# Kernel tuning notes

Measured on AMD Instinct MI355X. Metric: run time of the kernel, lower is better.

Reference implementation:

```python
import jax, jax.numpy as jnp
import numpy as np

H, NH, KVH = 2048, 16, 4
HD = H // NH            # 128
GROUPS = NH // KVH      # 4
E, TOPK = 8, 2
I_MOE, I_SH = 1408, 5632
THETA = 1000000.0
EPS = 1e-6
B, S = 1, 1024


def rms_norm(x, w):
    var = jnp.mean(jnp.square(x), axis=-1, keepdims=True)
    return x * jax.lax.rsqrt(var + EPS) * w


def rotate_half(x):
    x1, x2 = jnp.split(x, 2, axis=-1)
    return jnp.concatenate([-x2, x1], axis=-1)


def apply_rope(q, k, position_ids):
    # q: [B,S,NH,HD], k: [B,S,KVH,HD]
    inv_freq = 1.0 / (THETA ** (jnp.arange(0, HD, 2, dtype=jnp.float32) / HD))
    ang = position_ids.astype(jnp.float32)[..., None] * inv_freq  # [B,S,HD/2]
    emb = jnp.concatenate([ang, ang], axis=-1)                    # [B,S,HD]
    cos = jnp.cos(emb)[:, :, None, :]
    sin = jnp.sin(emb)[:, :, None, :]
    q = q * cos + rotate_half(q) * sin
    k = k * cos + rotate_half(k) * sin
    return q, k


def setup_inputs() -> dict:
    key = jax.random.key(0)
    ks = jax.random.split(key, 24)
    sd = 0.02
    inp = {
        "hidden_states": jax.random.normal(ks[0], (B, S, H), jnp.float32),
        "position_ids": jnp.arange(S, dtype=jnp.int32)[None, :].repeat(B, 0),
        "ln1_w": jnp.ones((H,), jnp.float32),
        "ln2_w": jnp.ones((H,), jnp.float32),
        "q_w": jax.random.normal(ks[1], (H, NH * HD), jnp.float32) * sd,
        "q_b": jnp.zeros((NH * HD,), jnp.float32),
        "k_w": jax.random.normal(ks[2], (H, KVH * HD), jnp.float32) * sd,
        "k_b": jnp.zeros((KVH * HD,), jnp.float32),
        "v_w": jax.random.normal(ks[3], (H, KVH * HD), jnp.float32) * sd,
        "v_b": jnp.zeros((KVH * HD,), jnp.float32),
        "o_w": jax.random.normal(ks[4], (NH * HD, H), jnp.float32) * sd,
        "router_w": jax.random.normal(ks[5], (H, E), jnp.float32) * sd,
        "e_gate": jax.random.normal(ks[6], (E, H, I_MOE), jnp.float32) * sd,
        "e_up": jax.random.normal(ks[7], (E, H, I_MOE), jnp.float32) * sd,
        "e_down": jax.random.normal(ks[8], (E, I_MOE, H), jnp.float32) * sd,
        "s_gate": jax.random.normal(ks[9], (H, I_SH), jnp.float32) * sd,
        "s_up": jax.random.normal(ks[10], (H, I_SH), jnp.float32) * sd,
        "s_down": jax.random.normal(ks[11], (I_SH, H), jnp.float32) * sd,
        "sg_w": jax.random.normal(ks[12], (H, 1), jnp.float32) * sd,
    }
    return inp


def attention(x, position_ids, q_w, q_b, k_w, k_b, v_w, v_b, o_w):
    b, s, _ = x.shape
    q = (x @ q_w + q_b).reshape(b, s, NH, HD)
    k = (x @ k_w + k_b).reshape(b, s, KVH, HD)
    v = (x @ v_w + v_b).reshape(b, s, KVH, HD)
    q, k = apply_rope(q, k, position_ids)
    # GQA: repeat kv heads
    k = jnp.repeat(k, GROUPS, axis=2)  # [b,s,NH,HD]
    v = jnp.repeat(v, GROUPS, axis=2)
    scale = HD ** -0.5
    scores = jnp.einsum("bqhd,bkhd->bhqk", q, k) * scale
    causal = jnp.tril(jnp.ones((s, s), bool))
    scores = jnp.where(causal[None, None], scores, jnp.finfo(scores.dtype).min)
    probs = jax.nn.softmax(scores, axis=-1)
    out = jnp.einsum("bhqk,bkhd->bqhd", probs, v).reshape(b, s, NH * HD)
    return out @ o_w


def sparse_moe(x, router_w, e_gate, e_up, e_down, s_gate, s_up, s_down, sg_w):
    b, s, h = x.shape
    xf = x.reshape(b * s, h)  # [T,H]
    T = b * s
    probs = jax.nn.softmax(xf @ router_w, axis=-1)        # [T,E]
    top_w, top_i = jax.lax.top_k(probs, TOPK)             # norm_topk_prob=False
    weights = jnp.zeros((T, E), xf.dtype).at[jnp.arange(T)[:, None], top_i].set(top_w)
    g = jax.nn.silu(jnp.einsum("th,ehi->eti", xf, e_gate))
    u = jnp.einsum("th,ehi->eti", xf, e_up)
    d = jnp.einsum("eti,eih->eth", g * u, e_down)         # [E,T,H]
    moe_out = jnp.einsum("eth,te->th", d, weights)
    shared = (jax.nn.silu(xf @ s_gate) * (xf @ s_up)) @ s_down
    shared = shared * jax.nn.sigmoid(xf @ sg_w)
    return (moe_out + shared).reshape(b, s, h)


def reference(hidden_states, position_ids, ln1_w, ln2_w, q_w, q_b, k_w, k_b,
              v_w, v_b, o_w, router_w, e_gate, e_up, e_down,
              s_gate, s_up, s_down, sg_w):
    h = hidden_states
    attn = attention(rms_norm(h, ln1_w), position_ids,
                     q_w, q_b, k_w, k_b, v_w, v_b, o_w)
    h = h + attn
    moe = sparse_moe(rms_norm(h, ln2_w), router_w, e_gate, e_up, e_down,
                     s_gate, s_up, s_down, sg_w)
    return h + moe
```

## Files before the change

kernel.cpp:

```cpp
#include <hip/hip_runtime.h>
#include <hip/hip_bf16.h>

#define S_ 1024
#define H_ 2048
#define NH_ 16
#define KVH_ 4
#define HD_ 128
#define IM_ 1408
#define ISH_ 5632
#define E_ 8

typedef __bf16 bf16x8 __attribute__((ext_vector_type(8)));
typedef float f32x4 __attribute__((ext_vector_type(4)));

typedef unsigned int __attribute__((address_space(1))) as1_u32;
typedef unsigned int __attribute__((address_space(3))) as3_u32;

__device__ __forceinline__ void gload16(const void* g, void* l) {
  __builtin_amdgcn_global_load_lds((const as1_u32*)g, (as3_u32*)l, 16, 0, 0);
}

__device__ __forceinline__ short f2bf(float f) {
  unsigned u = __float_as_uint(f);
  u = u + 0x7FFFu + ((u >> 16) & 1u);
  return (short)(u >> 16);
}

__device__ __forceinline__ f32x4 mfma16(bf16x8 a, bf16x8 b, f32x4 c) {
  return __builtin_amdgcn_mfma_f32_16x16x32_bf16(a, b, c, 0, 0, 0);
}

template<bool MAXOP>
__device__ __forceinline__ float block_reduce(float v, float* sbuf) {
  #pragma unroll
  for (int o = 32; o >= 1; o >>= 1) {
    float t = __shfl_down(v, o);
    v = MAXOP ? fmaxf(v, t) : (v + t);
  }
  int lane = threadIdx.x & 63, w = threadIdx.x >> 6;
  if (lane == 0) sbuf[w] = v;
  __syncthreads();
  float r = sbuf[0];
  #pragma unroll
  for (int i = 1; i < 4; i++) r = MAXOP ? fmaxf(r, sbuf[i]) : (r + sbuf[i]);
  __syncthreads();
  return r;
}

struct TransDesc {
  const float* src; short* dst;
  int R, C, tx, perz, base;
  long long srcZ, dstZ;
};
struct TransAll { TransDesc d[10]; };

#define TGRP 1096

__global__ __launch_bounds__(256) void mega_k(TransAll ta, int transBlocks,
                                              const int* pos_ids, float* ct, float* st,
                                              const float* qb, const float* kb, const float* vb,
                                              float* biasCat, int* counts,
                                              const float* hidden, const float* ln1_w,
                                              short* x1) {
  __shared__ float tile[4 * TGRP];
  __shared__ float sbuf[4];
  const int bid = blockIdx.x;
  const int t = threadIdx.x;
  if (bid < transBlocks) {
    int w = 0;
    #pragma unroll
    for (int i = 1; i < 10; i++) if (bid >= ta.d[i].base) w = i;
    const TransDesc& D = ta.d[w];
    int local = bid - D.base;
    int z = local / D.perz, rem = local - z * D.perz;
    int by = rem / D.tx, bx = rem - by * D.tx;
    const float* src = D.src + (long long)z * D.srcZ;
    short* dst = D.dst + (long long)z * D.dstZ;
    const int r0 = by * 64, c0 = bx * 64;
    const int C = D.C, R = D.R;
    #pragma unroll
    for (int i = 0; i < 4; i++) {
      int idx = t + i * 256;
      int row = idx >> 4, c4 = (idx & 15) * 4;
      f32x4 v = __builtin_nontemporal_load(
          (const f32x4*)&src[(size_t)(r0 + row) * C + c0 + c4]);
      *(f32x4*)&tile[(row >> 4) * TGRP + (row & 15) * 68 + c4] = v;
    }
    __syncthreads();
    const int col = t >> 2, seg = t & 3;
    const float* tp = &tile[seg * TGRP + col];
    short outv[16];
    #pragma unroll
    for (int j = 0; j < 16; j++)
      outv[j] = f2bf(tp[j * 68]);
    short* dp = &dst[(size_t)(c0 + col) * R + r0 + seg * 16];
    *(int4*)dp = *(const int4*)&outv[0];
    *(int4*)(dp + 8) = *(const int4*)&outv[8];
  } else if (bid < transBlocks + 256) {
    int pb = bid - transBlocks;
    if (pb == 0) {
      if (t < 16) counts[t] = 0;
      for (int j = t; j < 3072; j += 256)
        biasCat[j] = (j < 2048) ? qb[j] : ((j < 2560) ? kb[j - 2048] : vb[j - 2560]);
    }
    int i = pb * 256 + t;
    int p = i >> 6, f = i & 63;
    float pos = (float)pos_ids[p];
    float inv = powf(1.0e6f, -(float)f * (1.f / 64.f));
    float a = pos * inv;
    ct[i] = cosf(a); st[i] = sinf(a);
  } else {
    int tr = bid - transBlocks - 256;
    const float* xr = hidden + (long long)tr * H_;
    float ss = 0.f;
    for (int i = t; i < H_ / 4; i += 256) {
      float4 v = ((const float4*)xr)[i];
      ss += v.x * v.x + v.y * v.y + v.z * v.z + v.w * v.w;
    }
    ss = block_reduce<false>(ss, sbuf);
    float rs = rsqrtf(ss * (1.f / (float)H_) + 1e-6f);
    for (int i = t; i < H_; i += 256) {
      float xv = xr[i];
      x1[(long long)tr * H_ + i] = f2bf(xv * rs * ln1_w[i]);
    }
  }
}

struct GemmP {
  const short* A; long long strideA; int adiv; int lda;
  const short* B; long long strideB; int bdiv; int ldb;
  void* C; long long strideC; long long kstrideC; int cdiv; int ldc;
  const int* e_off; const int* e_cnt;
  const int* list; const float* scale;
  float alpha;
  int M, N, K;
  int cskip, ckb;
  int ksplit, kchunk;
  int upoff;
};

template<int EPI>
__device__ __forceinline__ void gemm_body(const GemmP& p, int bx, int by, int bz,
                                          short* As, short* Bs) {
  constexpr bool FUSED = (EPI == 6 || EPI == 7);
  constexpr bool GATH  = (EPI == 7);
  constexpr int BM = 128, BK = 32;
  const int zo = bz / p.ksplit;
  const int kc = bz - zo * p.ksplit;
  const int m0 = by * BM;
  const int n0 = bx * (FUSED ? 64 : 128);
  if (FUSED && n0 >= p.N) return;

  int off = 0, cnt = p.M;
  if constexpr (EPI == 4 || GATH) {
    off = p.e_off[zo]; cnt = p.e_cnt[zo];
    if (m0 >= cnt) return;
  }
  if (p.cskip && n0 >= m0 + BM) return;
  int kend = p.ckb ? min(m0 + BM, p.K) : p.K;
  const int kbeg = kc * p.kchunk;
  kend = min(kend, kbeg + p.kchunk);
  if (kbeg >= kend) return;

  const short* Ab = p.A + (long long)(zo / p.adiv) * p.strideA;
  const short* Bb = p.B + (long long)(zo / p.bdiv) * p.strideB;

  const int tid = threadIdx.x;
  const int lane = tid & 63, wid = tid >> 6;
  const int wr = wid >> 1, wc = wid & 1;
  const int kg = lane >> 4, li = lane & 15;

  const int srow = tid >> 2;
  const int scol = (((tid & 3) ^ ((tid >> 3) & 3))) * 8;
  const short* aSrc[2];
  const short* bSrc[2];
  #pragma unroll
  for (int c = 0; c < 2; c++) {
    int ra = srow + c * 64;
    int gr;
    if constexpr (GATH)          { int rr = m0 + ra; if (rr >= cnt) rr = cnt - 1; gr = p.list[off + rr]; }
    else if constexpr (EPI == 4) { int rr = m0 + ra; if (rr >= cnt) rr = cnt - 1; gr = off + rr; }
    else                         gr = m0 + ra;
    aSrc[c] = Ab + (long long)gr * p.lda + scol;
    int br = FUSED ? (n0 + srow + (c ? p.upoff : 0)) : (n0 + srow + c * 64);
    bSrc[c] = Bb + (long long)br * p.ldb + scol;
  }

  f32x4 acc[4][4];
  #pragma unroll
  for (int i = 0; i < 4; i++)
    #pragma unroll
    for (int j = 0; j < 4; j++) acc[i][j] = (f32x4){0.f, 0.f, 0.f, 0.f};

  #pragma unroll
  for (int c = 0; c < 2; c++) {
    gload16(aSrc[c] + kbeg, &As[tid * 8 + c * 2048]);
    gload16(bSrc[c] + kbeg, &Bs[tid * 8 + c * 2048]);
  }
  __syncthreads();

  const int kgx = kg ^ ((li >> 1) & 3);
  int brow[4];
  #pragma unroll
  for (int nj = 0; nj < 4; nj++)
    brow[nj] = FUSED ? (((nj & 2) ? 64 : 0) + wc * 32 + (nj & 1) * 16 + li)
                     : (wc * 64 + nj * 16 + li);

  int cur = 0;
  for (int k0 = kbeg; k0 < kend; k0 += BK) {
    const int nk = k0 + BK;
    if (nk < kend) {
      #pragma unroll
      for (int c = 0; c < 2; c++) {
        gload16(aSrc[c] + nk, &As[(cur ^ 1) * 4096 + tid * 8 + c * 2048]);
        gload16(bSrc[c] + nk, &Bs[(cur ^ 1) * 4096 + tid * 8 + c * 2048]);
      }
    }
    bf16x8 av[4], bv[4];
    #pragma unroll
    for (int mi = 0; mi < 4; mi++)
      av[mi] = *(const bf16x8*)&As[cur * 4096 + (wr * 64 + mi * 16 + li) * BK + kgx * 8];
    #pragma unroll
    for (int nj = 0; nj < 4; nj++)
      bv[nj] = *(const bf16x8*)&Bs[cur * 4096 + brow[nj] * BK + kgx * 8];
    #pragma unroll
    for (int mi = 0; mi < 4; mi++)
      #pragma unroll
      for (int nj = 0; nj < 4; nj++)
        acc[mi][nj] = mfma16(av[mi], bv[nj], acc[mi][nj]);
    __syncthreads();
    cur ^= 1;
  }

  const long long zc = (long long)(zo / p.cdiv) * p.strideC;
  if constexpr (FUSED) {
    short* C = (short*)p.C;
    #pragma unroll
    for (int mi = 0; mi < 4; mi++) {
      #pragma unroll
      for (int nj = 0; nj < 2; nj++) {
        #pragma unroll
        for (int r = 0; r < 4; r++) {
          int ml = wr * 64 + mi * 16 + kg * 4 + r;
          int mg = m0 + ml;
          int ng = n0 + wc * 32 + nj * 16 + li;
          float g = acc[mi][nj][r], u = acc[mi][nj + 2][r];
          float gu = g * (1.f / (1.f + __expf(-g))) * u;
          if constexpr (GATH) {
            if (mg < cnt) C[(long long)(off + mg) * p.ldc + ng] = f2bf(gu);
          } else {
            C[(long long)mg * p.ldc + ng] = f2bf(gu);
          }
        }
      }
    }
  } else {
    #pragma unroll
    for (int mi = 0; mi < 4; mi++) {
      #pragma unroll
      for (int nj = 0; nj < 4; nj++) {
        #pragma unroll
        for (int r = 0; r < 4; r++) {
          int ml = wr * 64 + mi * 16 + kg * 4 + r;
          int nl2 = wc * 64 + nj * 16 + li;
          int mg = m0 + ml, ng = n0 + nl2;
          float v = acc[mi][nj][r] * p.alpha;
          if constexpr (EPI == 0) {
            float* C = (float*)p.C + zc + (long long)kc * p.kstrideC;
            C[(long long)mg * p.ldc + ng] = v;
          } else if constexpr (EPI == 2) {
            short* C = (short*)p.C + zc;
            C[(long long)mg * p.ldc + ng] = f2bf(v);
          } else if constexpr (EPI == 4) {
            if (mg < cnt) {
              float* C = (float*)p.C;
              int tok = p.list[off + mg];
              atomicAdd(&C[(long long)tok * p.ldc + ng], p.scale[off + mg] * v);
            }
          } else if constexpr (EPI == 5) {
            float* C = (float*)p.C;
            atomicAdd(&C[(long long)mg * p.ldc + ng], p.scale[mg] * v);
          }
        }
      }
    }
  }
}

template<int EPI>
__global__ __launch_bounds__(256) void gemm_bt(GemmP p) {
  __shared__ __align__(16) short As[2 * 128 * 32];
  __shared__ __align__(16) short Bs[2 * 128 * 32];
  gemm_body<EPI>(p, blockIdx.x, blockIdx.y, blockIdx.z, As, Bs);
}

__global__ __launch_bounds__(256) void gemm_gu_dual(GemmP pe, GemmP ps) {
  __shared__ __align__(16) short As[2 * 128 * 32];
  __shared__ __align__(16) short Bs[2 * 128 * 32];
  int z = blockIdx.z;
  if (z < E_) gemm_body<7>(pe, blockIdx.x, blockIdx.y, z, As, Bs);
  else        gemm_body<6>(ps, (z - E_) * 22 + blockIdx.x, blockIdx.y, 0, As, Bs);
}

template<int EPI1, int EPI2>
__global__ __launch_bounds__(256) void gemm_dual(GemmP p1, GemmP p2, int z1) {
  __shared__ __align__(16) short As[2 * 128 * 32];
  __shared__ __align__(16) short Bs[2 * 128 * 32];
  int z = blockIdx.z;
  if (z < z1) gemm_body<EPI1>(p1, blockIdx.x, blockIdx.y, z, As, Bs);
  else        gemm_body<EPI2>(p2, blockIdx.x, blockIdx.y, z - z1, As, Bs);
}

__global__ __launch_bounds__(256) void rope_fused_k(const float* p0, const float* p1,
                                                    const float* bias, short* qr, short* kr,
                                                    short* vt, const float* ct, const float* st) {
  int i = blockIdx.x * 256 + threadIdx.x;
  if (i < 2097152) {
    int t = i >> 11, j = i & 2047;
    int d = j & 127, f = d & 63;
    float c = ct[t * 64 + f], s = st[t * 64 + f];
    long long base = (long long)t * 3072;
    float xv = p0[base + j] + p1[base + j] + bias[j];
    int jo = (d < 64) ? j + 64 : j - 64;
    float ov = p0[base + jo] + p1[base + jo] + bias[jo];
    if (d < 64) ov = -ov;
    qr[i] = f2bf(xv * c + ov * s);
  } else if (i < 2621440) {
    int j = i - 2097152;
    int t = j >> 9, jj = j & 511;
    int d = jj & 127, f = d & 63;
    float c = ct[t * 64 + f], s = st[t * 64 + f];
    long long base = (long long)t * 3072 + 2048;
    float xv = p0[base + jj] + p1[base + jj] + bias[2048 + jj];
    int jo = (d < 64) ? jj + 64 : jj - 64;
    float ov = p0[base + jo] + p1[base + jo] + bias[2048 + jo];
    if (d < 64) ov = -ov;
    kr[j] = f2bf(xv * c + ov * s);
  } else {
    int j = i - 2621440;
    int kvh = j >> 17, rem = j & 131071;
    int d = rem >> 10, s_ = rem & 1023;
    long long idx = (long long)s_ * 3072 + 2560 + kvh * 128 + d;
    vt[j] = f2bf(p0[idx] + p1[idx] + bias[2560 + kvh * 128 + d]);
  }
}

__global__ __launch_bounds__(256) void pv_red_k(const float* pp, short* attn) {
  int i = blockIdx.x * 256 + threadIdx.x;
  int r = i >> 11;
  int nl = r >> 8;
  float s = pp[i];
  for (int kc = 1; kc <= nl; kc++) s += pp[(size_t)kc * S_ * H_ + i];
  attn[i] = f2bf(s);
}

__global__ __launch_bounds__(256) void rmsnorm2f_k(const float* p0, const float* p1,
                                                   const float* hid, const float* w,
                                                   short* x2, float* outp, float* rs_out) {
  __shared__ float rowbuf[H_];
  __shared__ float sbuf[4];
  int tr = blockIdx.x;
  long long base = (long long)tr * H_;
  float ss = 0.f;
  for (int i = threadIdx.x; i < H_; i += 256) {
    float hv = p0[base + i] + p1[base + i] + hid[base + i];
    rowbuf[i] = hv;
    ss += hv * hv;
  }
  ss = block_reduce<false>(ss, sbuf);
  float rs = rsqrtf(ss * (1.f / (float)H_) + 1e-6f);
  for (int i = threadIdx.x; i < H_; i += 256) {
    float hv = rowbuf[i];
    outp[base + i] = hv;
    x2[base + i] = f2bf(hv * rs * w[i]);
  }
  if (threadIdx.x == 0) rs_out[tr] = rs;
}

__global__ __launch_bounds__(256) void softmax_k(const float* sc, short* P) {
  __shared__ float sbuf[4];
  long long row = blockIdx.x;
  int q = (int)(row & (S_ - 1));
  const float* sr = sc + row * S_;
  short* pr = P + row * S_;
  int L = q + 1;
  int Lcap = (q & ~127) + 128;
  float mx = -3.4e38f;
  for (int i = threadIdx.x; i < L; i += 256) mx = fmaxf(mx, sr[i]);
  mx = block_reduce<true>(mx, sbuf);
  float s = 0.f;
  for (int i = threadIdx.x; i < L; i += 256) s += __expf(sr[i] - mx);
  s = block_reduce<false>(s, sbuf);
  float inv = 1.f / s;
  for (int i = threadIdx.x; i < Lcap; i += 256) {
    float pv = (i < L) ? __expf(sr[i] - mx) * inv : 0.f;
    pr[i] = f2bf(pv);
  }
}

__global__ void router_k(const float* h2, const float* rs, const float* w2,
                         const float* rw, const float* sgw,
                         int* top_i, float* top_w, float* sg_sig, int* counts) {
  int t = blockIdx.x;
  int l = threadIdx.x;
  float le[8] = {0, 0, 0, 0, 0, 0, 0, 0};
  float ls = 0.f;
  float r = rs[t];
  for (int k = l; k < H_; k += 64) {
    float xv = h2[(long long)t * H_ + k] * r * w2[k];
    ls += xv * sgw[k];
    const float* rk = rw + k * E_;
    #pragma unroll
    for (int e = 0; e < E_; e++) le[e] += xv * rk[e];
  }
  #pragma unroll
  for (int o = 32; o >= 1; o >>= 1) {
    ls += __shfl_down(ls, o);
    #pragma unroll
    for (int e = 0; e < E_; e++) le[e] += __shfl_down(le[e], o);
  }
  if (l == 0) {
    float m = le[0];
    for (int e = 1; e < E_; e++) m = fmaxf(m, le[e]);
    float pe[8], s = 0.f;
    for (int e = 0; e < E_; e++) { pe[e] = __expf(le[e] - m); s += pe[e]; }
    float inv = 1.f / s;
    for (int e = 0; e < E_; e++) pe[e] *= inv;
    int i1 = 0;
    for (int e = 1; e < E_; e++) if (pe[e] > pe[i1]) i1 = e;
    int i2 = -1;
    for (int e = 0; e < E_; e++) if (e != i1 && (i2 < 0 || pe[e] > pe[i2])) i2 = e;
    top_i[2 * t] = i1; top_i[2 * t + 1] = i2;
    top_w[2 * t] = pe[i1]; top_w[2 * t + 1] = pe[i2];
    sg_sig[t] = 1.f / (1.f + __expf(-ls));
    atomicAdd(&counts[i1], 1); atomicAdd(&counts[i2], 1);
  }
}

__global__ void scan_k(const int* counts, int* offs) {
  if (threadIdx.x == 0 && blockIdx.x == 0) {
    int s = 0;
    for (int e = 0; e < E_; e++) { offs[e] = s; s += counts[e]; }
  }
}

__global__ __launch_bounds__(256) void fill_k(const int* top_i, const float* top_w, const int* offs,
                                              int* pos, int* list, float* pw) {
  int t = blockIdx.x * 256 + threadIdx.x;
  if (t >= S_) return;
  for (int j = 0; j < 2; j++) {
    int e = top_i[2 * t + j];
    int p_ = atomicAdd(&pos[e], 1);
    int slot = offs[e] + p_;
    list[slot] = t; pw[slot] = top_w[2 * t + j];
  }
}

static GemmP mkp() {
  GemmP p{};
  p.adiv = 1; p.bdiv = 1; p.cdiv = 1; p.alpha = 1.f;
  p.ksplit = 1; p.kchunk = 1 << 30;
  p.upoff = 0; p.kstrideC = 0;
  return p;
}

extern "C" void kernel_launch(void* const* d_in, const int* in_sizes, int n_in,
                              void* d_out, int out_size, void* d_ws, size_t ws_size,
                              hipStream_t stream) {
  const float* hidden   = (const float*)d_in[0];
  const int*   pos_ids  = (const int*)d_in[1];
  const float* ln1_w    = (const float*)d_in[2];
  const float* ln2_w    = (const float*)d_in[3];
  const float* q_w      = (const float*)d_in[4];
  const float* q_b      = (const float*)d_in[5];
  const float* k_w      = (const float*)d_in[6];
  const float* k_b      = (const float*)d_in[7];
  const float* v_w      = (const float*)d_in[8];
  const float* v_b      = (const float*)d_in[9];
  const float* o_w      = (const float*)d_in[10];
  const float* router_w = (const float*)d_in[11];
  const float* e_gate   = (const float*)d_in[12];
  const float* e_up     = (const float*)d_in[13];
  const float* e_down   = (const float*)d_in[14];
  const float* s_gate   = (const float*)d_in[15];
  const float* s_up     = (const float*)d_in[16];
  const float* s_down   = (const float*)d_in[17];
  const float* sg_w     = (const float*)d_in[18];
  float* out = (float*)d_out;

  char* base = (char*)d_ws;
  size_t off_ = 0;
  auto alc = [&](size_t nbytes) -> char* {
    off_ = (off_ + 255) & ~(size_t)255;
    char* p = base + off_;
    off_ += nbytes;
    return p;
  };
  short* qkvT = (short*)alc((size_t)3072 * H_ * 2);
  short* oT   = (short*)alc((size_t)H_ * H_ * 2);
  short* eguT = (short*)alc((size_t)E_ * 2816 * H_ * 2);
  short* edT  = (short*)alc((size_t)E_ * H_ * IM_ * 2);
  short* sguT = (short*)alc((size_t)11264 * H_ * 2);
  short* sdT  = (short*)alc((size_t)H_ * ISH_ * 2);
  short* x1      = (short*)alc((size_t)S_ * H_ * 2);
  float* qkv_p   = (float*)alc((size_t)2 * S_ * 3072 * 4);
  float* o_part  = (float*)alc((size_t)2 * S_ * H_ * 4);
  float* pv_part = (float*)alc((size_t)4 * S_ * H_ * 4);
  float* biasCat = (float*)alc(3072 * 4);
  float* ct      = (float*)alc((size_t)S_ * 64 * 4);
  float* st      = (float*)alc((size_t)S_ * 64 * 4);
  short* qr      = (short*)alc((size_t)S_ * H_ * 2);
  short* kr      = (short*)alc((size_t)S_ * 512 * 2);
  short* vt      = (short*)alc((size_t)S_ * 512 * 2);
  short* attn    = (short*)alc((size_t)S_ * H_ * 2);
  short* x2      = (short*)alc((size_t)S_ * H_ * 2);
  float* rs2     = (float*)alc(S_ * 4);
  int*   top_i   = (int*)alc(2 * S_ * 4);
  float* top_w   = (float*)alc(2 * S_ * 4);
  float* sg_sig  = (float*)alc(S_ * 4);
  int*   counts  = (int*)alc(64);
  int*   pos     = counts + 8;
  int*   offs    = (int*)alc(32);
  int*   list    = (int*)alc(2 * S_ * 4);
  float* pw      = (float*)alc(2 * S_ * 4);
  char*  region  = alc(100663296);
  float* scores  = (float*)region;
  short* P       = (short*)(region + 67108864);
  short* gu_moeB = (short*)region;
  short* gushB   = (short*)(region + 16777216);

  {
    TransAll ta{};
    int b = 0;
    auto add = [&](int i, const float* s, short* d, int R, int C, int tz,
                   long long sZ, long long dZ) {
      int tx = C / 64, ty = R / 64;
      ta.d[i] = TransDesc{s, d, R, C, tx, tx * ty, b, sZ, dZ};
      b += tx * ty * tz;
    };
    add(0, q_w, qkvT, H_, H_, 1, 0, 0);
    add(1, k_w, qkvT + (size_t)2048 * H_, H_, 512, 1, 0, 0);
    add(2, v_w, qkvT + (size_t)2560 * H_, H_, 512, 1, 0, 0);
    add(3, o_w, oT, H_, H_, 1, 0, 0);
    add(4, e_gate, eguT, H_, IM_, E_, (long long)H_ * IM_, (long long)2816 * H_);
    add(5, e_up, eguT + (size_t)1408 * H_, H_, IM_, E_, (long long)H_ * IM_, (long long)2816 * H_);
    add(6, e_down, edT, IM_, H_, E_, (long long)IM_ * H_, (long long)IM_ * H_);
    add(7, s_gate, sguT, H_, ISH_, 1, 0, 0);
    add(8, s_up, sguT + (size_t)5632 * H_, H_, ISH_, 1, 0, 0);
    add(9, s_down, sdT, ISH_, H_, 1, 0, 0);
    mega_k<<<b + 256 + 1024, 256, 0, stream>>>(ta, b, pos_ids, ct, st, q_b, k_b, v_b,
                                               biasCat, counts, hidden, ln1_w, x1);
  }

  {
    GemmP p = mkp();
    p.A = x1; p.lda = H_;
    p.B = qkvT; p.ldb = H_;
    p.C = qkv_p; p.kstrideC = (long long)S_ * 3072; p.ldc = 3072;
    p.M = S_; p.N = 3072; p.K = H_;
    p.ksplit = 2; p.kchunk = 1024;
    gemm_bt<0><<<dim3(24, 8, 2), 256, 0, stream>>>(p);
  }

  rope_fused_k<<<12288, 256, 0, stream>>>(qkv_p, qkv_p + (size_t)S_ * 3072, biasCat,
                                          qr, kr, vt, ct, st);

  {
    GemmP p = mkp();
    p.A = qr; p.strideA = HD_; p.lda = H_;
    p.B = kr; p.strideB = HD_; p.bdiv = 4; p.ldb = 512;
    p.C = scores; p.strideC = (long long)S_ * S_; p.ldc = S_;
    p.alpha = 0.08838834764831845f;
    p.M = S_; p.N = S_; p.K = HD_; p.cskip = 1;
    gemm_bt<0><<<dim3(8, 8, NH_), 256, 0, stream>>>(p);
  }
  softmax_k<<<NH_ * S_, 256, 0, stream>>>(scores, P);
  {
    GemmP p = mkp();
    p.A = P; p.strideA = (long long)S_ * S_; p.lda = S_;
    p.B = vt; p.strideB = (long long)HD_ * S_; p.bdiv = 4; p.ldb = S_;
    p.C = pv_part; p.strideC = HD_; p.kstrideC = (long long)S_ * H_; p.ldc = H_;
    p.M = S_; p.N = HD_; p.K = S_; p.ckb = 1;
    p.ksplit = 4; p.kchunk = 256;
    gemm_bt<0><<<dim3(1, 8, NH_ * 4), 256, 0, stream>>>(p);
  }
  pv_red_k<<<8192, 256, 0, stream>>>(pv_part, attn);
  {
    GemmP p = mkp();
    p.A = attn; p.lda = H_;
    p.B = oT; p.ldb = H_;
    p.C = o_part; p.kstrideC = (long long)S_ * H_; p.ldc = H_;
    p.M = S_; p.N = H_; p.K = H_;
    p.ksplit = 2; p.kchunk = 1024;
    gemm_bt<0><<<dim3(16, 8, 2), 256, 0, stream>>>(p);
  }

  rmsnorm2f_k<<<S_, 256, 0, stream>>>(o_part, o_part + (size_t)S_ * H_, hidden,
                                      ln2_w, x2, out, rs2);

  router_k<<<S_, 64, 0, stream>>>(out, rs2, ln2_w, router_w, sg_w, top_i, top_w, sg_sig, counts);
  scan_k<<<1, 1, 0, stream>>>(counts, offs);
  fill_k<<<4, 256, 0, stream>>>(top_i, top_w, offs, pos, list, pw);

  {
    GemmP pe = mkp();
    pe.A = x2; pe.lda = H_;
    pe.B = eguT; pe.strideB = (long long)2816 * H_; pe.ldb = H_;
    pe.C = gu_moeB; pe.ldc = IM_;
    pe.e_off = offs; pe.e_cnt = counts; pe.list = list;
    pe.M = S_; pe.N = IM_; pe.K = H_;
    pe.upoff = IM_;
    GemmP ps = mkp();
    ps.A = x2; ps.lda = H_;
    ps.B = sguT; ps.ldb = H_;
    ps.C = gushB; ps.ldc = ISH_;
    ps.M = S_; ps.N = ISH_; ps.K = H_;
    ps.upoff = ISH_;
    gemm_gu_dual<<<dim3(22, 8, 12), 256, 0, stream>>>(pe, ps);
  }

  {
    GemmP pe = mkp();
    pe.A = gu_moeB; pe.lda = IM_;
    pe.B = edT; pe.strideB = (long long)H_ * IM_; pe.ldb = IM_;
    pe.C = out; pe.ldc = H_;
    pe.e_off = offs; pe.e_cnt = counts; pe.list = list; pe.scale = pw;
    pe.M = S_; pe.N = H_; pe.K = IM_;
    pe.ksplit = 2; pe.kchunk = 704;
    GemmP ps = mkp();
    ps.A = gushB; ps.lda = ISH_;
    ps.B = sdT; ps.ldb = ISH_;
    ps.C = out; ps.ldc = H_; ps.scale = sg_sig;
    ps.M = S_; ps.N = H_; ps.K = ISH_;
    ps.ksplit = 4; ps.kchunk = 1408;
    gemm_dual<4, 5><<<dim3(16, 8, E_ * 2 + 4), 256, 0, stream>>>(pe, ps, E_ * 2);
  }
}
```

Measured before the change: 555.9 us.

## Overlap MoE weight transposes with attention GEMMs by co-launching blocks

Result: faster. 537.4 us (-3.3%).

```diff
diff --git a/kernel.cpp b/kernel.cpp
--- a/kernel.cpp
+++ b/kernel.cpp
@@ -52,11 +52,40 @@
   int R, C, tx, perz, base;
   long long srcZ, dstZ;
 };
-struct TransAll { TransDesc d[10]; };
+struct TransAttn { TransDesc d[4]; };
+struct TransMoE  { TransDesc d[6]; };
 
 #define TGRP 1096
 
-__global__ __launch_bounds__(256) void mega_k(TransAll ta, int transBlocks,
+__device__ __forceinline__ void trans_body(const TransDesc& D, int local, float* tile) {
+  const int t = threadIdx.x;
+  int z = local / D.perz, rem = local - z * D.perz;
+  int by = rem / D.tx, bx = rem - by * D.tx;
+  const float* src = D.src + (long long)z * D.srcZ;
+  short* dst = D.dst + (long long)z * D.dstZ;
+  const int r0 = by * 64, c0 = bx * 64;
+  const int C = D.C, R = D.R;
+  #pragma unroll
+  for (int i = 0; i < 4; i++) {
+    int idx = t + i * 256;
+    int row = idx >> 4, c4 = (idx & 15) * 4;
+    f32x4 v = __builtin_nontemporal_load(
+        (const f32x4*)&src[(size_t)(r0 + row) * C + c0 + c4]);
+    *(f32x4*)&tile[(row >> 4) * TGRP + (row & 15) * 68 + c4] = v;
+  }
+  __syncthreads();
+  const int col = t >> 2, seg = t & 3;
+  const float* tp = &tile[seg * TGRP + col];
+  short outv[16];
+  #pragma unroll
+  for (int j = 0; j < 16; j++)
+    outv[j] = f2bf(tp[j * 68]);
+  short* dp = &dst[(size_t)(c0 + col) * R + r0 + seg * 16];
+  *(int4*)dp = *(const int4*)&outv[0];
+  *(int4*)(dp + 8) = *(const int4*)&outv[8];
+}
+
+__global__ __launch_bounds__(256) void mega_k(TransAttn ta, int transBlocks,
                                               const int* pos_ids, float* ct, float* st,
                                               const float* qb, const float* kb, const float* vb,
                                               float* biasCat, int* counts,
@@ -69,33 +98,8 @@
   if (bid < transBlocks) {
     int w = 0;
     #pragma unroll
-    for (int i = 1; i < 10; i++) if (bid >= ta.d[i].base) w = i;
-    const TransDesc& D = ta.d[w];
-    int local = bid - D.base;
-    int z = local / D.perz, rem = local - z * D.perz;
-    int by = rem / D.tx, bx = rem - by * D.tx;
-    const float* src = D.src + (long long)z * D.srcZ;
-    short* dst = D.dst + (long long)z * D.dstZ;
-    const int r0 = by * 64, c0 = bx * 64;
-    const int C = D.C, R = D.R;
-    #pragma unroll
-    for (int i = 0; i < 4; i++) {
-      int idx = t + i * 256;
-      int row = idx >> 4, c4 = (idx & 15) * 4;
-      f32x4 v = __builtin_nontemporal_load(
-          (const f32x4*)&src[(size_t)(r0 + row) * C + c0 + c4]);
-      *(f32x4*)&tile[(row >> 4) * TGRP + (row & 15) * 68 + c4] = v;
-    }
-    __syncthreads();
-    const int col = t >> 2, seg = t & 3;
-    const float* tp = &tile[seg * TGRP + col];
-    short outv[16];
-    #pragma unroll
-    for (int j = 0; j < 16; j++)
-      outv[j] = f2bf(tp[j * 68]);
-    short* dp = &dst[(size_t)(c0 + col) * R + r0 + seg * 16];
-    *(int4*)dp = *(const int4*)&outv[0];
-    *(int4*)(dp + 8) = *(const int4*)&outv[8];
+    for (int i = 1; i < 4; i++) if (bid >= ta.d[i].base) w = i;
+    trans_body(ta.d[w], bid - ta.d[w].base, tile);
   } else if (bid < transBlocks + 256) {
     int pb = bid - transBlocks;
     if (pb == 0) {
@@ -292,6 +296,25 @@
   __shared__ __align__(16) short As[2 * 128 * 32];
   __shared__ __align__(16) short Bs[2 * 128 * 32];
   gemm_body<EPI>(p, blockIdx.x, blockIdx.y, blockIdx.z, As, Bs);
+}
+
+template<int EPI>
+__global__ __launch_bounds__(256) void gemm_tr(GemmP p, TransMoE tm, int zsplit,
+                                               int tbase, int tcount) {
+  __shared__ __align__(16) short smem[2 * 128 * 32 * 2];
+  const int bz = blockIdx.z;
+  if (bz >= zsplit) {
+    int idx = (bz - zsplit) * (gridDim.x * gridDim.y) + blockIdx.x + gridDim.x * blockIdx.y;
+    if (idx < tcount) {
+      int g = tbase + idx;
+      int w = 0;
+      #pragma unroll
+      for (int i = 1; i < 6; i++) if (g >= tm.d[i].base) w = i;
+      trans_body(tm.d[w], g - tm.d[w].base, (float*)smem);
+    }
+    return;
+  }
+  gemm_body<EPI>(p, blockIdx.x, blockIdx.y, bz, smem, smem + 2 * 128 * 32);
 }
 
 __global__ __launch_bounds__(256) void gemm_gu_dual(GemmP pe, GemmP ps) {
@@ -529,25 +552,38 @@
   short* gu_moeB = (short*)region;
   short* gushB   = (short*)(region + 16777216);
 
-  {
-    TransAll ta{};
+  TransMoE tm{};
+  int tb = 0;
+  {
+    auto addm = [&](int i, const float* s, short* d, int R, int C, int tz,
+                    long long sZ, long long dZ) {
+      int tx = C / 64, ty = R / 64;
+      tm.d[i] = TransDesc{s, d, R, C, tx, tx * ty, tb, sZ, dZ};
+      tb += tx * ty * tz;
+    };
+    addm(0, e_gate, eguT, H_, IM_, E_, (long long)H_ * IM_, (long long)2816 * H_);
+    addm(1, e_up, eguT + (size_t)1408 * H_, H_, IM_, E_, (long long)H_ * IM_, (long long)2816 * H_);
+    addm(2, e_down, edT, IM_, H_, E_, (long long)IM_ * H_, (long long)IM_ * H_);
+    addm(3, s_gate, sguT, H_, ISH_, 1, 0, 0);
+    addm(4, s_up, sguT + (size_t)5632 * H_, H_, ISH_, 1, 0, 0);
+    addm(5, s_down, sdT, ISH_, H_, 1, 0, 0);
+  }
+  const int T_QKV = 12096;
+  const int T_SC  = 6528;
+  const int T_O   = tb - T_QKV - T_SC;
+
+  {
+    TransAttn ta{};
     int b = 0;
-    auto add = [&](int i, const float* s, short* d, int R, int C, int tz,
-                   long long sZ, long long dZ) {
+    auto add = [&](int i, const float* s, short* d, int R, int C) {
       int tx = C / 64, ty = R / 64;
-      ta.d[i] = TransDesc{s, d, R, C, tx, tx * ty, b, sZ, dZ};
-      b += tx * ty * tz;
+      ta.d[i] = TransDesc{s, d, R, C, tx, tx * ty, b, 0, 0};
+      b += tx * ty;
     };
-    add(0, q_w, qkvT, H_, H_, 1, 0, 0);
-    add(1, k_w, qkvT + (size_t)2048 * H_, H_, 512, 1, 0, 0);
-    add(2, v_w, qkvT + (size_t)2560 * H_, H_, 512, 1, 0, 0);
-    add(3, o_w, oT, H_, H_, 1, 0, 0);
-    add(4, e_gate, eguT, H_, IM_, E_, (long long)H_ * IM_, (long long)2816 * H_);
-    add(5, e_up, eguT + (size_t)1408 * H_, H_, IM_, E_, (long long)H_ * IM_, (long long)2816 * H_);
-    add(6, e_down, edT, IM_, H_, E_, (long long)IM_ * H_, (long long)IM_ * H_);
-    add(7, s_gate, sguT, H_, ISH_, 1, 0, 0);
-    add(8, s_up, sguT + (size_t)5632 * H_, H_, ISH_, 1, 0, 0);
-    add(9, s_down, sdT, ISH_, H_, 1, 0, 0);
+    add(0, q_w, qkvT, H_, H_);
+    add(1, k_w, qkvT + (size_t)2048 * H_, H_, 512);
+    add(2, v_w, qkvT + (size_t)2560 * H_, H_, 512);
+    add(3, o_w, oT, H_, H_);
     mega_k<<<b + 256 + 1024, 256, 0, stream>>>(ta, b, pos_ids, ct, st, q_b, k_b, v_b,
                                                biasCat, counts, hidden, ln1_w, x1);
   }
@@ -559,7 +595,7 @@
     p.C = qkv_p; p.kstrideC = (long long)S_ * 3072; p.ldc = 3072;
     p.M = S_; p.N = 3072; p.K = H_;
     p.ksplit = 2; p.kchunk = 1024;
-    gemm_bt<0><<<dim3(24, 8, 2), 256, 0, stream>>>(p);
+    gemm_tr<0><<<dim3(24, 8, 2 + 63), 256, 0, stream>>>(p, tm, 2, 0, T_QKV);
   }
 
   rope_fused_k<<<12288, 256, 0, stream>>>(qkv_p, qkv_p + (size_t)S_ * 3072, biasCat,
@@ -572,7 +608,7 @@
     p.C = scores; p.strideC = (long long)S_ * S_; p.ldc = S_;
     p.alpha = 0.08838834764831845f;
     p.M = S_; p.N = S_; p.K = HD_; p.cskip = 1;
-    gemm_bt<0><<<dim3(8, 8, NH_), 256, 0, stream>>>(p);
+    gemm_tr<0><<<dim3(8, 8, NH_ + 102), 256, 0, stream>>>(p, tm, NH_, T_QKV, T_SC);
   }
   softmax_k<<<NH_ * S_, 256, 0, stream>>>(scores, P);
   {
@@ -592,7 +628,7 @@
     p.C = o_part; p.kstrideC = (long long)S_ * H_; p.ldc = H_;
     p.M = S_; p.N = H_; p.K = H_;
     p.ksplit = 2; p.kchunk = 1024;
-    gemm_bt<0><<<dim3(16, 8, 2), 256, 0, stream>>>(p);
+    gemm_tr<0><<<dim3(16, 8, 2 + 53), 256, 0, stream>>>(p, tm, 2, T_QKV + T_SC, T_O);
   }
 
   rmsnorm2f_k<<<S_, 256, 0, stream>>>(o_part, o_part + (size_t)S_ * H_, hidden,
```
